# Optimization experiments

Hardware: AMD Instinct MI355X
Metric: run time of the kernel (lower is better)

The kernel has to match this reference:

```python
import jax, jax.numpy as jnp
import numpy as np

B, N, H, R, L = 32, 512, 768, 5, 2
FF = 2 * H  # ffn expansion = hidden_size * 2
LN_EPS = 1e-5


def layer_norm(x, g, b):
    mu = jnp.mean(x, axis=-1, keepdims=True)
    var = jnp.mean(jnp.square(x - mu), axis=-1, keepdims=True)
    return (x - mu) * jax.lax.rsqrt(var + LN_EPS) * g + b


def setup_inputs() -> dict:
    key = jax.random.key(0)
    ks = jax.random.split(key, 20)
    s = 1.0 / np.sqrt(H)
    inp = {
        'node_embeddings': jax.random.normal(ks[0], (B, N, H), jnp.float32),
        'relation_graph': jax.random.uniform(ks[1], (B, R, N, N), jnp.float32),
        # stacked per-layer params (leading dim = L layers)
        'rel_W': jax.random.normal(ks[2], (L, R, H, H), jnp.float32) * s,
        'rel_b': jax.random.normal(ks[3], (L, R, H), jnp.float32) * s,
        'gate_W': jax.random.normal(ks[4], (L, H, R), jnp.float32) * s,
        'gate_b': jax.random.normal(ks[5], (L, R), jnp.float32) * s,
        'out_W': jax.random.normal(ks[6], (L, H, H), jnp.float32) * s,
        'out_b': jax.random.normal(ks[7], (L, H), jnp.float32) * s,
        'ln1_g': jnp.ones((L, H), jnp.float32),
        'ln1_b': jnp.zeros((L, H), jnp.float32),
        'ffn_W1': jax.random.normal(ks[8], (L, H, FF), jnp.float32) * s,
        'ffn_b1': jax.random.normal(ks[9], (L, FF), jnp.float32) * s,
        'ffn_W2': jax.random.normal(ks[10], (L, FF, H), jnp.float32) * (1.0 / np.sqrt(FF)),
        'ffn_b2': jax.random.normal(ks[11], (L, H), jnp.float32) * s,
        'ln2_g': jnp.ones((L, H), jnp.float32),
        'ln2_b': jnp.zeros((L, H), jnp.float32),
    }
    return inp


def reference(node_embeddings, relation_graph, rel_W, rel_b, gate_W, gate_b,
              out_W, out_b, ln1_g, ln1_b, ffn_W1, ffn_b1, ffn_W2, ffn_b2,
              ln2_g, ln2_b):
    adj = relation_graph.astype(jnp.float32)            # [B,R,N,N]
    deg = jnp.clip(jnp.sum(adj, axis=-1, keepdims=True), 1.0)  # [B,R,N,1]
    x = node_embeddings
    rw_collect = []
    for l in range(rel_W.shape[0]):  # small fixed layer count
        # per-relation degree-normalized aggregation + linear + relu
        agg = jnp.einsum('brnm,bmh->brnh', adj, x) / deg           # [B,R,N,H]
        msg = jax.nn.relu(jnp.einsum('brnh,rhd->brnd', agg, rel_W[l])
                          + rel_b[l][None, :, None, :])            # [B,R,N,H]
        # softmax gate over relations from mean-pooled nodes
        pooled = jnp.mean(x, axis=1)                                # [B,H]
        logits = pooled @ gate_W[l] + gate_b[l]                     # [B,R]
        w = jax.nn.softmax(logits, axis=-1)
        merged = jnp.einsum('brnd,br->bnd', msg, w)                 # [B,N,H]
        merged = merged @ out_W[l] + out_b[l]                       # dropout=identity (eval)
        hidden = layer_norm(x + merged, ln1_g[l], ln1_b[l])
        ff = jax.nn.relu(hidden @ ffn_W1[l] + ffn_b1[l]) @ ffn_W2[l] + ffn_b2[l]
        x = layer_norm(hidden + ff, ln2_g[l], ln2_b[l])
        rw_collect.append(jnp.mean(w, axis=0))
    relation_weights_stat = jnp.mean(jnp.stack(rw_collect, axis=0), axis=0)  # [R]
    return x, relation_weights_stat
```

## Files before the change

kernel.cpp:

```cpp
#include <hip/hip_runtime.h>
#include <hip/hip_bf16.h>
#include <math.h>

#define Bdim 32
#define Ndim 512
#define Hdim 768
#define Rdim 5
#define Ldim 2
#define FFdim 1536
#define LN_EPS 1e-5f

typedef __attribute__((ext_vector_type(8))) __bf16 bf16x8;
typedef __attribute__((ext_vector_type(8))) unsigned short ushort8;
typedef __attribute__((ext_vector_type(4))) float f32x4;

__device__ __forceinline__ unsigned short f2bf(float f) {
  union { float f; unsigned int u; } x;
  x.f = f;
  unsigned int u = x.u;
  return (unsigned short)((u + 0x7FFFu + ((u >> 16) & 1u)) >> 16);
}

__device__ __forceinline__ void gload_lds16(const unsigned short* g, unsigned short* l) {
  __builtin_amdgcn_global_load_lds(
      (const __attribute__((address_space(1))) void*)g,
      (__attribute__((address_space(3))) void*)l, 16, 0, 0);
}

template <int EPI, bool OUT_BF16, int NSEG>
__global__ __launch_bounds__(256) void mfma_gemm(
    const unsigned short* __restrict__ A, long sA, long sA2, int lda,
    const unsigned short* __restrict__ Bt, long sB, int ldb,
    void* __restrict__ Cp, long sC, int ldc,
    int segK, long segA, long segB,
    const float* __restrict__ bias,
    const float* __restrict__ resid,
    const float* __restrict__ wv) {
  __shared__ __align__(16) unsigned short As0[128 * 32];
  __shared__ __align__(16) unsigned short Bs0[128 * 32];
  __shared__ __align__(16) unsigned short As1[128 * 32];
  __shared__ __align__(16) unsigned short Bs1[128 * 32];

  const int gx = gridDim.x, gy = gridDim.y;
  int lin = blockIdx.x + gx * (blockIdx.y + gy * blockIdx.z);
  {
    const int total = gx * gy * gridDim.z;
    const int q = total >> 3, r8 = total & 7;
    const int xcd = lin & 7, slot = lin >> 3;
    lin = (xcd < r8) ? (xcd * (q + 1) + slot)
                     : (r8 * (q + 1) + (xcd - r8) * q + slot);
  }
  const int bx = lin % gx;
  const int t2 = lin / gx;
  const int by = t2 % gy;
  const int zb = t2 / gy;

  const int zlo = zb & 31;
  const int zhi = zb >> 5;
  const int row0 = by * 128;
  const int col0 = bx * 128;
  const int tid = threadIdx.x;
  const int wid = tid >> 6;
  const int lane = tid & 63;
  const int mq = (wid & 1) * 64;
  const int nq = (wid >> 1) * 64;
  const int lr = lane & 15;
  const int lk = (lane >> 4) * 8;

  const int c0 = wid * 2;
  const int srow0 = c0 * 16 + (lane >> 2);
  const int se = (lane & 3) * 8;

  const unsigned short* Ag0 =
      A + (long)zlo * sA + (long)zhi * sA2 + (long)(row0 + srow0) * lda + se;
  const unsigned short* Ag1 = Ag0 + (long)16 * lda;
  const unsigned short* Bg0 = Bt + (long)zlo * sB + (long)(col0 + srow0) * ldb + se;
  const unsigned short* Bg1 = Bg0 + (long)16 * ldb;

  f32x4 acc[4][4];
  f32x4 acc2[4][4];
#pragma unroll
  for (int i = 0; i < 4; i++)
#pragma unroll
    for (int j = 0; j < 4; j++) {
      acc[i][j] = (f32x4){0.f, 0.f, 0.f, 0.f};
      if (EPI == 1) acc2[i][j] = (f32x4){0.f, 0.f, 0.f, 0.f};
    }

  const int spseg = segK >> 5;
  const int nsteps = NSEG * spseg;
  int sseg = 0, sk = 0;

  auto stage = [&](unsigned short* Asl, unsigned short* Bsl) {
    const long ao = (long)sseg * segA + sk;
    const long bo = (long)sseg * segB + sk;
    gload_lds16(Ag0 + ao, Asl + c0 * 512);
    gload_lds16(Ag1 + ao, Asl + c0 * 512 + 512);
    gload_lds16(Bg0 + bo, Bsl + c0 * 512);
    gload_lds16(Bg1 + bo, Bsl + c0 * 512 + 512);
    sk += 32;
    if (sk == segK) { sk = 0; sseg++; }
  };

  auto compute = [&](const unsigned short* Asb, const unsigned short* Bsb) {
    bf16x8 af[4], bfr[4];
#pragma unroll
    for (int i = 0; i < 4; i++) af[i] = *(const bf16x8*)&Asb[(mq + i * 16 + lr) * 32 + lk];
#pragma unroll
    for (int j = 0; j < 4; j++) bfr[j] = *(const bf16x8*)&Bsb[(nq + j * 16 + lr) * 32 + lk];
#pragma unroll
    for (int i = 0; i < 4; i++)
#pragma unroll
      for (int j = 0; j < 4; j++)
        acc[i][j] = __builtin_amdgcn_mfma_f32_16x16x32_bf16(af[i], bfr[j], acc[i][j], 0, 0, 0);
  };

  int cnt = 0, cseg = 0;
  auto fold = [&]() {
    const float wval = wv[(row0 >> 9) * Rdim + cseg];
#pragma unroll
    for (int j = 0; j < 4; j++) {
      const float bj = bias[cseg * Hdim + col0 + nq + j * 16 + lr];
#pragma unroll
      for (int i = 0; i < 4; i++)
#pragma unroll
        for (int rr = 0; rr < 4; rr++) {
          acc2[i][j][rr] += wval * fmaxf(acc[i][j][rr] + bj, 0.f);
          acc[i][j][rr] = 0.f;
        }
    }
    cseg++;
  };

  stage(As0, Bs0);
  __syncthreads();

  for (int s = 0; s < nsteps; s += 2) {
    if (s + 1 < nsteps) stage(As1, Bs1);
    compute(As0, Bs0);
    if (EPI == 1 && ++cnt == spseg) { fold(); cnt = 0; }
    __syncthreads();
    if (s + 1 < nsteps) {
      if (s + 2 < nsteps) stage(As0, Bs0);
      compute(As1, Bs1);
      if (EPI == 1 && ++cnt == spseg) { fold(); cnt = 0; }
      __syncthreads();
    }
  }

  float bvals[4];
  if (EPI == 2 || EPI == 3) {
#pragma unroll
    for (int j = 0; j < 4; j++) bvals[j] = bias[col0 + nq + j * 16 + lr];
  }

  float* Cf = (float*)Cp;
  unsigned short* Ch = (unsigned short*)Cp;
  const long Coff = (long)zb * sC;

#pragma unroll
  for (int i = 0; i < 4; i++) {
#pragma unroll
    for (int r = 0; r < 4; r++) {
      const int grow = row0 + mq + i * 16 + (lane >> 4) * 4 + r;
#pragma unroll
      for (int j = 0; j < 4; j++) {
        const int gcol = col0 + nq + j * 16 + lr;
        const long cidx = Coff + (long)grow * ldc + gcol;
        float v;
        if (EPI == 1) v = acc2[i][j][r];
        else v = acc[i][j][r];
        if (EPI == 2) v += bvals[j] + resid[cidx];
        if (EPI == 3) v = fmaxf(v + bvals[j], 0.f);
        if (OUT_BF16) Ch[cidx] = f2bf(v);
        else Cf[cidx] = v;
      }
    }
  }
}

__global__ __launch_bounds__(256) void transpose_cvt(
    const float* __restrict__ in, unsigned short* __restrict__ out, int R_, int C_) {
  __shared__ float t[32][33];
  const int z = blockIdx.z;
  const float* ib = in + (long)z * R_ * C_;
  unsigned short* ob = out + (long)z * R_ * C_;
  const int r0 = blockIdx.y * 32, c0 = blockIdx.x * 32;
  const int tx = threadIdx.x & 31, ty = threadIdx.x >> 5;
#pragma unroll
  for (int i = 0; i < 4; i++)
    t[ty + i * 8][tx] = ib[(long)(r0 + ty + i * 8) * C_ + c0 + tx];
  __syncthreads();
#pragma unroll
  for (int i = 0; i < 4; i++)
    ob[(long)(c0 + ty + i * 8) * R_ + r0 + tx] = f2bf(t[tx][ty + i * 8]);
}

__global__ __launch_bounds__(256) void norm_adj_kernel(const float* __restrict__ adj,
                                                       unsigned short* __restrict__ out,
                                                       long total_rows) {
  const long w = ((long)blockIdx.x * 256 + threadIdx.x) >> 6;
  const int lane = threadIdx.x & 63;
  if (w >= total_rows) return;
  const float* row = adj + w * Ndim;
  float4 f0 = *(const float4*)(row + lane * 8);
  float4 f1 = *(const float4*)(row + lane * 8 + 4);
  float s = f0.x + f0.y + f0.z + f0.w + f1.x + f1.y + f1.z + f1.w;
#pragma unroll
  for (int off = 32; off; off >>= 1) s += __shfl_xor(s, off, 64);
  const float inv = 1.0f / fmaxf(s, 1.0f);
  ushort8 o = {f2bf(f0.x * inv), f2bf(f0.y * inv), f2bf(f0.z * inv), f2bf(f0.w * inv),
               f2bf(f1.x * inv), f2bf(f1.y * inv), f2bf(f1.z * inv), f2bf(f1.w * inv)};
  *(ushort8*)&out[w * Ndim + lane * 8] = o;
}

__global__ __launch_bounds__(256) void pool_kernel(const float* __restrict__ x,
                                                   float* __restrict__ part) {
  const int ch = blockIdx.x, b = blockIdx.y, t = threadIdx.x;
  const float* xb = x + ((long)b * Ndim + ch * 64) * Hdim;
  float s0 = 0.f, s1 = 0.f, s2 = 0.f;
  for (int n = 0; n < 64; n++) {
    const float* r = xb + (long)n * Hdim;
    s0 += r[t]; s1 += r[t + 256]; s2 += r[t + 512];
  }
  float* p = part + ((long)b * 8 + ch) * Hdim;
  p[t] = s0; p[t + 256] = s1; p[t + 512] = s2;
}

__global__ void gate_kernel(const float* __restrict__ part,
                            const float* __restrict__ gW,
                            const float* __restrict__ gb,
                            float* __restrict__ w_out) {
  __shared__ float pooled[Hdim];
  __shared__ float logits[Rdim];
  const int b = blockIdx.x;
  const int h = threadIdx.x;
  float s = 0.f;
#pragma unroll
  for (int c = 0; c < 8; c++) s += part[((long)b * 8 + c) * Hdim + h];
  pooled[h] = s * (1.0f / Ndim);
  __syncthreads();
  if (h < Rdim) {
    float acc = gb[h];
    for (int k = 0; k < Hdim; k++) acc += pooled[k] * gW[k * Rdim + h];
    logits[h] = acc;
  }
  __syncthreads();
  if (h == 0) {
    float mx = -1e30f;
    for (int r = 0; r < Rdim; r++) mx = fmaxf(mx, logits[r]);
    float e[Rdim];
    float se = 0.f;
    for (int r = 0; r < Rdim; r++) { e[r] = expf(logits[r] - mx); se += e[r]; }
    for (int r = 0; r < Rdim; r++) w_out[b * Rdim + r] = e[r] / se;
  }
}

__global__ __launch_bounds__(256) void ln_kernel(
    const float* __restrict__ X,
    const float* __restrict__ g, const float* __restrict__ bb,
    float* __restrict__ out, unsigned short* __restrict__ out_bf) {
  __shared__ float red[8];
  const long base = (long)blockIdx.x * Hdim;
  const int t = threadIdx.x;
  float v0 = X[base + t];
  float v1 = X[base + t + 256];
  float v2 = X[base + t + 512];
  float s = v0 + v1 + v2;
  float ss = v0 * v0 + v1 * v1 + v2 * v2;
#pragma unroll
  for (int off = 32; off > 0; off >>= 1) {
    s += __shfl_down(s, off, 64);
    ss += __shfl_down(ss, off, 64);
  }
  const int wid = t >> 6;
  if ((t & 63) == 0) { red[wid] = s; red[4 + wid] = ss; }
  __syncthreads();
  s = red[0] + red[1] + red[2] + red[3];
  ss = red[4] + red[5] + red[6] + red[7];
  const float mu = s * (1.0f / Hdim);
  const float var = ss * (1.0f / Hdim) - mu * mu;
  const float inv = rsqrtf(var + LN_EPS);
  const float o0 = (v0 - mu) * inv * g[t] + bb[t];
  const float o1 = (v1 - mu) * inv * g[t + 256] + bb[t + 256];
  const float o2 = (v2 - mu) * inv * g[t + 512] + bb[t + 512];
  out[base + t] = o0;
  out[base + t + 256] = o1;
  out[base + t + 512] = o2;
  if (out_bf) {
    out_bf[base + t] = f2bf(o0);
    out_bf[base + t + 256] = f2bf(o1);
    out_bf[base + t + 512] = f2bf(o2);
  }
}

__global__ void stat_kernel(const float* __restrict__ w_buf, float* __restrict__ out) {
  const int r = threadIdx.x;
  if (r < Rdim) {
    float s = 0.f;
    for (int l = 0; l < Ldim; l++)
      for (int b = 0; b < Bdim; b++) s += w_buf[l * Bdim * Rdim + b * Rdim + r];
    out[r] = s * (1.0f / (Ldim * Bdim));
  }
}

extern "C" void kernel_launch(void* const* d_in, const int* in_sizes, int n_in,
                              void* d_out, int out_size, void* d_ws, size_t ws_size,
                              hipStream_t stream) {
  const float* node = (const float*)d_in[0];
  const float* adj  = (const float*)d_in[1];
  const float* relW = (const float*)d_in[2];
  const float* relb = (const float*)d_in[3];
  const float* gateW = (const float*)d_in[4];
  const float* gateb = (const float*)d_in[5];
  const float* outW = (const float*)d_in[6];
  const float* outb = (const float*)d_in[7];
  const float* ln1g = (const float*)d_in[8];
  const float* ln1b = (const float*)d_in[9];
  const float* fW1 = (const float*)d_in[10];
  const float* fb1 = (const float*)d_in[11];
  const float* fW2 = (const float*)d_in[12];
  const float* fb2 = (const float*)d_in[13];
  const float* ln2g = (const float*)d_in[14];
  const float* ln2b = (const float*)d_in[15];

  const long BNH = (long)Bdim * Ndim * Hdim;
  const long BRNN = (long)Bdim * Rdim * Ndim * Ndim;
  float* xout = (float*)d_out;
  float* stat = xout + BNH;

  float* ws = (float*)d_ws;
  float* hidden = ws;
  float* tmp    = ws + BNH;
  unsigned short* agg_all = (unsigned short*)(ws + 2 * BNH);
  unsigned short* xT_bf = agg_all + Rdim * BNH;
  unsigned short* merged_bf = xT_bf + BNH;
  unsigned short* adjn_bf = merged_bf + BNH;
  unsigned short* relWT = adjn_bf + BRNN;
  unsigned short* outWT = relWT + (long)Ldim * Rdim * Hdim * Hdim;
  unsigned short* W1T = outWT + (long)Ldim * Hdim * Hdim;
  unsigned short* W2T = W1T + (long)Ldim * Hdim * FFdim;
  float* w_buf = (float*)(W2T + (long)Ldim * FFdim * Hdim);
  float* part = w_buf + Ldim * Bdim * Rdim;
  unsigned short* hidden_bf = xT_bf;
  unsigned short* ffh_bf = (unsigned short*)tmp;
  float* tmp2 = (float*)agg_all;

  {
    const long rows = (long)Bdim * Rdim * Ndim;
    norm_adj_kernel<<<(int)(rows / 4), 256, 0, stream>>>(adj, adjn_bf, rows);
  }
  transpose_cvt<<<dim3(Hdim / 32, Hdim / 32, Ldim * Rdim), 256, 0, stream>>>(relW, relWT, Hdim, Hdim);
  transpose_cvt<<<dim3(Hdim / 32, Hdim / 32, Ldim), 256, 0, stream>>>(outW, outWT, Hdim, Hdim);
  transpose_cvt<<<dim3(FFdim / 32, Hdim / 32, Ldim), 256, 0, stream>>>(fW1, W1T, Hdim, FFdim);
  transpose_cvt<<<dim3(Hdim / 32, FFdim / 32, Ldim), 256, 0, stream>>>(fW2, W2T, FFdim, Hdim);

  for (int l = 0; l < Ldim; l++) {
    const float* xin = (l == 0) ? node : xout;

    pool_kernel<<<dim3(8, Bdim), 256, 0, stream>>>(xin, part);
    gate_kernel<<<Bdim, Hdim, 0, stream>>>(
        part, gateW + (long)l * Hdim * Rdim, gateb + (long)l * Rdim,
        w_buf + (long)l * Bdim * Rdim);

    transpose_cvt<<<dim3(Hdim / 32, Ndim / 32, Bdim), 256, 0, stream>>>(xin, xT_bf, Ndim, Hdim);

    mfma_gemm<0, true, 1><<<dim3(Hdim / 128, Ndim / 128, Bdim * Rdim), 256, 0, stream>>>(
        adjn_bf, (long)Rdim * Ndim * Ndim, (long)Ndim * Ndim, Ndim,
        xT_bf, (long)Hdim * Ndim, Ndim,
        agg_all, (long)Ndim * Hdim, Hdim,
        Ndim, 0, 0, nullptr, nullptr, nullptr);

    mfma_gemm<1, true, Rdim><<<dim3(Hdim / 128, (Bdim * Ndim) / 128, 1), 256, 0, stream>>>(
        agg_all, 0, 0, Hdim,
        relWT + (long)l * Rdim * Hdim * Hdim, 0, Hdim,
        merged_bf, 0, Hdim,
        Hdim, BNH, (long)Hdim * Hdim,
        relb + (long)l * Rdim * Hdim, nullptr,
        w_buf + (long)l * Bdim * Rdim);

    mfma_gemm<2, false, 1><<<dim3(Hdim / 128, (Bdim * Ndim) / 128, 1), 256, 0, stream>>>(
        merged_bf, 0, 0, Hdim,
        outWT + (long)l * Hdim * Hdim, 0, Hdim,
        tmp, 0, Hdim,
        Hdim, 0, 0,
        outb + (long)l * Hdim, xin, nullptr);

    ln_kernel<<<Bdim * Ndim, 256, 0, stream>>>(
        tmp, ln1g + (long)l * Hdim, ln1b + (long)l * Hdim, hidden, hidden_bf);

    mfma_gemm<3, true, 1><<<dim3(FFdim / 128, (Bdim * Ndim) / 128, 1), 256, 0, stream>>>(
        hidden_bf, 0, 0, Hdim,
        W1T + (long)l * Hdim * FFdim, 0, Hdim,
        ffh_bf, 0, FFdim,
        Hdim, 0, 0,
        fb1 + (long)l * FFdim, nullptr, nullptr);

    mfma_gemm<2, false, 1><<<dim3(Hdim / 128, (Bdim * Ndim) / 128, 1), 256, 0, stream>>>(
        ffh_bf, 0, 0, FFdim,
        W2T + (long)l * FFdim * Hdim, 0, FFdim,
        tmp2, 0, Hdim,
        FFdim, 0, 0,
        fb2 + (long)l * Hdim, hidden, nullptr);

    ln_kernel<<<Bdim * Ndim, 256, 0, stream>>>(
        tmp2, ln2g + (long)l * Hdim, ln2b + (long)l * Hdim, xout, nullptr);
  }

  stat_kernel<<<1, 64, 0, stream>>>(w_buf, stat);
}
```

Baseline: 1.493 ms.

## Triple-buffer GEMM LDS pipeline with explicit vmcnt waits and MFMA priority

Replaces the double-buffered LDS staging with a three-stage ring. Global-to-LDS loads run two tiles ahead, and explicit s_waitcnt vmcnt counts and raw barriers replace the __syncthreads pairs. Fragments are read into registers before the next stage is issued into the freed buffer, and s_setprio raises wave priority around the MFMA block. Launch bounds now request minimum occupancy per template variant. The aim is to hide global memory latency better, at the cost of 50% more LDS and fragile hand-tuned wait counts.

```diff
diff --git a/kernel.cpp b/kernel.cpp
--- a/kernel.cpp
+++ b/kernel.cpp
@@ -28,7 +28,7 @@
 }
 
 template <int EPI, bool OUT_BF16, int NSEG>
-__global__ __launch_bounds__(256) void mfma_gemm(
+__global__ __launch_bounds__(256, (EPI == 1) ? 2 : 3) void mfma_gemm(
     const unsigned short* __restrict__ A, long sA, long sA2, int lda,
     const unsigned short* __restrict__ Bt, long sB, int ldb,
     void* __restrict__ Cp, long sC, int ldc,
@@ -36,10 +36,8 @@
     const float* __restrict__ bias,
     const float* __restrict__ resid,
     const float* __restrict__ wv) {
-  __shared__ __align__(16) unsigned short As0[128 * 32];
-  __shared__ __align__(16) unsigned short Bs0[128 * 32];
-  __shared__ __align__(16) unsigned short As1[128 * 32];
-  __shared__ __align__(16) unsigned short Bs1[128 * 32];
+  __shared__ __align__(16) unsigned short As[3 * 128 * 32];
+  __shared__ __align__(16) unsigned short Bs[3 * 128 * 32];
 
   const int gx = gridDim.x, gy = gridDim.y;
   int lin = blockIdx.x + gx * (blockIdx.y + gy * blockIdx.z);
@@ -91,28 +89,17 @@
   const int nsteps = NSEG * spseg;
   int sseg = 0, sk = 0;
 
-  auto stage = [&](unsigned short* Asl, unsigned short* Bsl) {
+  auto stage = [&](int buf) {
+    unsigned short* Asl = As + buf * 4096 + c0 * 512;
+    unsigned short* Bsl = Bs + buf * 4096 + c0 * 512;
     const long ao = (long)sseg * segA + sk;
     const long bo = (long)sseg * segB + sk;
-    gload_lds16(Ag0 + ao, Asl + c0 * 512);
-    gload_lds16(Ag1 + ao, Asl + c0 * 512 + 512);
-    gload_lds16(Bg0 + bo, Bsl + c0 * 512);
-    gload_lds16(Bg1 + bo, Bsl + c0 * 512 + 512);
+    gload_lds16(Ag0 + ao, Asl);
+    gload_lds16(Ag1 + ao, Asl + 512);
+    gload_lds16(Bg0 + bo, Bsl);
+    gload_lds16(Bg1 + bo, Bsl + 512);
     sk += 32;
     if (sk == segK) { sk = 0; sseg++; }
-  };
-
-  auto compute = [&](const unsigned short* Asb, const unsigned short* Bsb) {
-    bf16x8 af[4], bfr[4];
-#pragma unroll
-    for (int i = 0; i < 4; i++) af[i] = *(const bf16x8*)&Asb[(mq + i * 16 + lr) * 32 + lk];
-#pragma unroll
-    for (int j = 0; j < 4; j++) bfr[j] = *(const bf16x8*)&Bsb[(nq + j * 16 + lr) * 32 + lk];
-#pragma unroll
-    for (int i = 0; i < 4; i++)
-#pragma unroll
-      for (int j = 0; j < 4; j++)
-        acc[i][j] = __builtin_amdgcn_mfma_f32_16x16x32_bf16(af[i], bfr[j], acc[i][j], 0, 0, 0);
   };
 
   int cnt = 0, cseg = 0;
@@ -132,20 +119,39 @@
     cseg++;
   };
 
-  stage(As0, Bs0);
-  __syncthreads();
-
-  for (int s = 0; s < nsteps; s += 2) {
-    if (s + 1 < nsteps) stage(As1, Bs1);
-    compute(As0, Bs0);
+  stage(0); stage(1); stage(2);
+
+  int buf = 0;
+  for (int s = 0; s < nsteps; ++s) {
+    const int rem = nsteps - s;
+    if (rem > 2)       asm volatile("s_waitcnt vmcnt(8)" ::: "memory");
+    else if (rem == 2) asm volatile("s_waitcnt vmcnt(4)" ::: "memory");
+    else               asm volatile("s_waitcnt vmcnt(0)" ::: "memory");
+    __builtin_amdgcn_s_barrier();
+
+    const unsigned short* Asb = As + buf * 4096;
+    const unsigned short* Bsb = Bs + buf * 4096;
+    bf16x8 af[4], bfr[4];
+#pragma unroll
+    for (int i = 0; i < 4; i++) af[i] = *(const bf16x8*)&Asb[(mq + i * 16 + lr) * 32 + lk];
+#pragma unroll
+    for (int j = 0; j < 4; j++) bfr[j] = *(const bf16x8*)&Bsb[(nq + j * 16 + lr) * 32 + lk];
+    asm volatile("s_waitcnt lgkmcnt(0)" ::: "memory");
+    __builtin_amdgcn_sched_barrier(0);
+    __builtin_amdgcn_s_barrier();
+
+    if (s + 3 < nsteps) stage(buf);
+
+    __builtin_amdgcn_s_setprio(1);
+#pragma unroll
+    for (int i = 0; i < 4; i++)
+#pragma unroll
+      for (int j = 0; j < 4; j++)
+        acc[i][j] = __builtin_amdgcn_mfma_f32_16x16x32_bf16(af[i], bfr[j], acc[i][j], 0, 0, 0);
+    __builtin_amdgcn_s_setprio(0);
+
     if (EPI == 1 && ++cnt == spseg) { fold(); cnt = 0; }
-    __syncthreads();
-    if (s + 1 < nsteps) {
-      if (s + 2 < nsteps) stage(As0, Bs0);
-      compute(As1, Bs1);
-      if (EPI == 1 && ++cnt == spseg) { fold(); cnt = 0; }
-      __syncthreads();
-    }
+    buf = (buf == 2) ? 0 : buf + 1;
   }
 
   float bvals[4];
```

New measurement: 1.365 ms. 1.09x faster.
